# Kernel optimization log

Hardware: AMD Instinct MI355X
Metric: run time of the kernel (lower is better)

Reference implementation:

```python
import jax, jax.numpy as jnp
import numpy as np

B, S, H, A = 2, 512, 256, 128


def setup_inputs() -> dict:
    key = jax.random.key(0)
    k1, k2, k3, k4 = jax.random.split(key, 4)
    x = jax.random.normal(k1, (B, S, H), dtype=jnp.float32)
    attention_mask = jax.random.randint(k2, (B, S), 0, 2, dtype=jnp.int32)
    # xavier_normal for w_a, standard normal for query (as in torch init)
    w_a = jax.random.normal(k3, (H, A), dtype=jnp.float32) * np.sqrt(2.0 / (H + A))
    query = jax.random.normal(k4, (A,), dtype=jnp.float32)
    return {"x": x, "attention_mask": attention_mask, "w_a": w_a, "query": query}


def reference(x, attention_mask, w_a, query):
    # attention_type == 'fixed' path of SelfAttention
    b, s, h = x.shape
    tri = jnp.tril(jnp.ones((s, s), dtype=x.dtype))  # tri[i,j]=1 iff j<=i (causal)
    # values[b,i,j,h] = x[b,j,h] if j<=i else 0  (the O(S^2*H) masked broadcast)
    values = tri[None, :, :, None] * x[:, None, :, :]          # (B,S,S,H)
    key_t = jnp.tanh(jnp.einsum('bijh,ha->bija', values, w_a))  # (B,S,S,A)
    temp = jnp.einsum('a,bija->bij', query, key_t)              # (B,S,S)
    # additive softmax mask: 0 on lower triangle, -inf above diagonal
    smask = jnp.where(tri == 1, 0.0, -jnp.inf).astype(x.dtype)
    d = jax.nn.softmax(temp + smask, axis=-1)                   # (B,S,S)
    am = (attention_mask[:, :s] != 0)
    pair = (am[:, :, None] & am[:, None, :]).astype(d.dtype)    # (B,S,S)
    d = d * pair
    a = jnp.einsum('bij,bjh->bih', d, x)                        # (B,S,H)
    return (a, d)
```

## Files before the change

kernel.cpp:

```cpp
#include <hip/hip_runtime.h>
#include <math.h>

#define BB 2
#define SS 512
#define HH 256
#define AA 128
#define CH 4
#define NCH (SS / CH)

__global__ void k_tc(const float* __restrict__ x,
                     const int* __restrict__ am,
                     const float* __restrict__ w_a,
                     const float* __restrict__ query,
                     float* __restrict__ Ews,
                     float* __restrict__ Cws) {
    const int blk  = blockIdx.x;
    const int b    = blk >> 7;
    const int c    = blk & 127;
    const int j0   = c * CH;
    const int tid  = threadIdx.x;
    const int a    = tid & 127;
    const int half = tid >> 7;

    __shared__ float xs[CH][HH];
    __shared__ float sred[CH][2][AA];
    __shared__ float Wl[CH];

    const float4* xr4 = (const float4*)(x + (size_t)(b * SS + j0) * HH);
    ((float4*)&xs[0][0])[tid] = xr4[tid];
    __syncthreads();

    float acc0 = 0.f, acc1 = 0.f, acc2 = 0.f, acc3 = 0.f;
    const int hbase = half * 128;
    for (int hh = 0; hh < 128; hh += 4) {
        const int h = hbase + hh;
        const float w0 = w_a[(h + 0) * AA + a];
        const float w1 = w_a[(h + 1) * AA + a];
        const float w2 = w_a[(h + 2) * AA + a];
        const float w3 = w_a[(h + 3) * AA + a];
        const float4 x0 = *(const float4*)&xs[0][h];
        const float4 x1 = *(const float4*)&xs[1][h];
        const float4 x2 = *(const float4*)&xs[2][h];
        const float4 x3 = *(const float4*)&xs[3][h];
        acc0 = fmaf(x0.x, w0, fmaf(x0.y, w1, fmaf(x0.z, w2, fmaf(x0.w, w3, acc0))));
        acc1 = fmaf(x1.x, w0, fmaf(x1.y, w1, fmaf(x1.z, w2, fmaf(x1.w, w3, acc1))));
        acc2 = fmaf(x2.x, w0, fmaf(x2.y, w1, fmaf(x2.z, w2, fmaf(x2.w, w3, acc2))));
        acc3 = fmaf(x3.x, w0, fmaf(x3.y, w1, fmaf(x3.z, w2, fmaf(x3.w, w3, acc3))));
    }
    sred[0][half][a] = acc0;
    sred[1][half][a] = acc1;
    sred[2][half][a] = acc2;
    sred[3][half][a] = acc3;
    __syncthreads();

    const int wvi  = tid >> 6;
    const int lane = tid & 63;
    {
        const int r = wvi;
        const float f0 = sred[r][0][lane]      + sred[r][1][lane];
        const float f1 = sred[r][0][lane + 64] + sred[r][1][lane + 64];
        float v = tanhf(f0) * query[lane] + tanhf(f1) * query[lane + 64];
        for (int off = 32; off > 0; off >>= 1)
            v += __shfl_down(v, off, 64);
        if (lane == 0) {
            const float e = expf(v);
            Wl[r] = am[b * SS + j0 + r] ? e : 0.f;
            Ews[b * SS + j0 + r] = e;
        }
    }
    __syncthreads();

    const float cacc = fmaf(Wl[0], xs[0][tid],
                       fmaf(Wl[1], xs[1][tid],
                       fmaf(Wl[2], xs[2][tid],
                            Wl[3] * xs[3][tid])));
    Cws[(size_t)(b * NCH + c) * HH + tid] = cacc;
}

__global__ void k_out(const float* __restrict__ Ews,
                      const float* __restrict__ Cws,
                      const int* __restrict__ am,
                      const float* __restrict__ x,
                      float* __restrict__ dout,
                      float* __restrict__ aout) {
    const int blk  = blockIdx.x;
    const int b    = blk >> 7;
    const int i0   = (blk & 127) << 2;
    const int tid  = threadIdx.x;
    const int lane = tid & 63;
    const int wvi  = tid >> 6;

    __shared__ float Es[SS];
    __shared__ float Ws[SS];
    __shared__ float red[4];
    __shared__ float Pinv[4];

    const float e0 = Ews[b * SS + tid];
    const float e1 = Ews[b * SS + tid + 256];
    const int  am0 = am[b * SS + tid];
    const int  am1 = am[b * SS + tid + 256];
    Es[tid] = e0;             Es[tid + 256] = e1;
    Ws[tid] = am0 ? e0 : 0.f; Ws[tid + 256] = am1 ? e1 : 0.f;

    float p = ((tid <= i0) ? e0 : 0.f) + ((tid + 256 <= i0) ? e1 : 0.f);
    for (int off = 32; off > 0; off >>= 1)
        p += __shfl_down(p, off, 64);
    if (lane == 0) red[wvi] = p;
    __syncthreads();
    if (tid == 0) {
        const float P0 = red[0] + red[1] + red[2] + red[3];
        const float P1 = P0 + Es[i0 + 1];
        const float P2 = P1 + Es[i0 + 2];
        const float P3 = P2 + Es[i0 + 3];
        Pinv[0] = 1.f / P0; Pinv[1] = 1.f / P1;
        Pinv[2] = 1.f / P2; Pinv[3] = 1.f / P3;
    }
    __syncthreads();

    const int* amg = am + b * SS;
    int ami[4];
#pragma unroll
    for (int r = 0; r < 4; ++r) ami[r] = amg[i0 + r];

    const size_t drow = (size_t)(b * SS + i0) * SS;
    const int c4  = tid & 127;
    const int jc  = c4 << 2;
    const float4 wv4 = *(const float4*)&Ws[jc];
#pragma unroll
    for (int pp = 0; pp < 2; ++pp) {
        const int   r  = (tid >> 7) + 2 * pp;
        const int   i  = i0 + r;
        const float pv = Pinv[r];
        const bool  on = ami[r] != 0;
        float4 o;
        o.x = (on && jc + 0 <= i) ? wv4.x * pv : 0.f;
        o.y = (on && jc + 1 <= i) ? wv4.y * pv : 0.f;
        o.z = (on && jc + 2 <= i) ? wv4.z * pv : 0.f;
        o.w = (on && jc + 3 <= i) ? wv4.w * pv : 0.f;
        *(float4*)&dout[drow + (size_t)r * SS + jc] = o;
    }

    const int nfull = i0 >> 2;
    const float* xb = x + (size_t)b * SS * HH + tid;
    const float* Cb = Cws + (size_t)b * NCH * HH + tid;

    float s0 = 0.f, s1 = 0.f, s2 = 0.f, s3 = 0.f;
    int cc = 0;
    for (; cc + 4 <= nfull; cc += 4) {
        s0 += Cb[(size_t)(cc + 0) * HH];
        s1 += Cb[(size_t)(cc + 1) * HH];
        s2 += Cb[(size_t)(cc + 2) * HH];
        s3 += Cb[(size_t)(cc + 3) * HH];
    }
    for (; cc < nfull; ++cc)
        s0 += Cb[(size_t)cc * HH];
    const float base = (s0 + s1) + (s2 + s3);

    const float a0v = fmaf(Ws[i0],     xb[(size_t)(i0)     * HH], base);
    const float a1v = fmaf(Ws[i0 + 1], xb[(size_t)(i0 + 1) * HH], a0v);
    const float a2v = fmaf(Ws[i0 + 2], xb[(size_t)(i0 + 2) * HH], a1v);
    const float a3v = fmaf(Ws[i0 + 3], xb[(size_t)(i0 + 3) * HH], a2v);

    const size_t arow = (size_t)(b * SS + i0) * HH + tid;
    const float av[4] = {a0v, a1v, a2v, a3v};
#pragma unroll
    for (int r = 0; r < 4; ++r)
        aout[arow + (size_t)r * HH] = ami[r] ? av[r] * Pinv[r] : 0.f;
}

extern "C" void kernel_launch(void* const* d_in, const int* in_sizes, int n_in,
                              void* d_out, int out_size, void* d_ws, size_t ws_size,
                              hipStream_t stream) {
    const float* x     = (const float*)d_in[0];
    const int*   am    = (const int*)d_in[1];
    const float* w_a   = (const float*)d_in[2];
    const float* query = (const float*)d_in[3];

    float* a_out  = (float*)d_out;
    float* d_outp = a_out + (size_t)BB * SS * HH;

    float* Ews = (float*)d_ws;
    float* Cws = Ews + BB * SS;

    k_tc <<<BB * NCH,    256, 0, stream>>>(x, am, w_a, query, Ews, Cws);
    k_out<<<BB * SS / 4, 256, 0, stream>>>(Ews, Cws, am, x, d_outp, a_out);
}
```

Baseline: 74.84 us.

## Fuse both kernels into one cooperative kernel with grid-wide prefix scans

Merges the projection kernel and the output kernel into a single cooperative launch of 256 blocks, separated by two grid syncs. Between the syncs, wavefronts compute parallel prefix sums over the chunk partial context vectors and over the exp weights. The output stage then reads one prefix value instead of looping over all earlier chunks and doing a per-block reduction for the softmax denominator. It also drops the shared-memory staging of x in favour of direct global float4 loads. In exchange it adds grid-sync overhead, depends on cooperative launch co-residency, and computes the denominator by prefix summation, which changes the floating-point ordering.

```diff
diff --git a/kernel.cpp b/kernel.cpp
--- a/kernel.cpp
+++ b/kernel.cpp
@@ -1,5 +1,8 @@
 #include <hip/hip_runtime.h>
+#include <hip/hip_cooperative_groups.h>
 #include <math.h>
+
+namespace cg = cooperative_groups;
 
 #define BB 2
 #define SS 512
@@ -8,164 +11,183 @@
 #define CH 4
 #define NCH (SS / CH)
 
-__global__ void k_tc(const float* __restrict__ x,
-                     const int* __restrict__ am,
-                     const float* __restrict__ w_a,
-                     const float* __restrict__ query,
-                     float* __restrict__ Ews,
-                     float* __restrict__ Cws) {
+__global__ __launch_bounds__(256)
+void k_all(const float* __restrict__ x,
+           const int* __restrict__ am,
+           const float* __restrict__ w_a,
+           const float* __restrict__ query,
+           float* __restrict__ Ews,
+           float* __restrict__ Cws,
+           float* __restrict__ Pws,
+           float* __restrict__ dout,
+           float* __restrict__ aout)
+{
+    cg::grid_group grid = cg::this_grid();
     const int blk  = blockIdx.x;
-    const int b    = blk >> 7;
-    const int c    = blk & 127;
-    const int j0   = c * CH;
-    const int tid  = threadIdx.x;
-    const int a    = tid & 127;
-    const int half = tid >> 7;
-
-    __shared__ float xs[CH][HH];
-    __shared__ float sred[CH][2][AA];
-    __shared__ float Wl[CH];
-
-    const float4* xr4 = (const float4*)(x + (size_t)(b * SS + j0) * HH);
-    ((float4*)&xs[0][0])[tid] = xr4[tid];
-    __syncthreads();
-
-    float acc0 = 0.f, acc1 = 0.f, acc2 = 0.f, acc3 = 0.f;
-    const int hbase = half * 128;
-    for (int hh = 0; hh < 128; hh += 4) {
-        const int h = hbase + hh;
-        const float w0 = w_a[(h + 0) * AA + a];
-        const float w1 = w_a[(h + 1) * AA + a];
-        const float w2 = w_a[(h + 2) * AA + a];
-        const float w3 = w_a[(h + 3) * AA + a];
-        const float4 x0 = *(const float4*)&xs[0][h];
-        const float4 x1 = *(const float4*)&xs[1][h];
-        const float4 x2 = *(const float4*)&xs[2][h];
-        const float4 x3 = *(const float4*)&xs[3][h];
-        acc0 = fmaf(x0.x, w0, fmaf(x0.y, w1, fmaf(x0.z, w2, fmaf(x0.w, w3, acc0))));
-        acc1 = fmaf(x1.x, w0, fmaf(x1.y, w1, fmaf(x1.z, w2, fmaf(x1.w, w3, acc1))));
-        acc2 = fmaf(x2.x, w0, fmaf(x2.y, w1, fmaf(x2.z, w2, fmaf(x2.w, w3, acc2))));
-        acc3 = fmaf(x3.x, w0, fmaf(x3.y, w1, fmaf(x3.z, w2, fmaf(x3.w, w3, acc3))));
-    }
-    sred[0][half][a] = acc0;
-    sred[1][half][a] = acc1;
-    sred[2][half][a] = acc2;
-    sred[3][half][a] = acc3;
-    __syncthreads();
-
-    const int wvi  = tid >> 6;
-    const int lane = tid & 63;
-    {
-        const int r = wvi;
-        const float f0 = sred[r][0][lane]      + sred[r][1][lane];
-        const float f1 = sred[r][0][lane + 64] + sred[r][1][lane + 64];
-        float v = tanhf(f0) * query[lane] + tanhf(f1) * query[lane + 64];
-        for (int off = 32; off > 0; off >>= 1)
-            v += __shfl_down(v, off, 64);
-        if (lane == 0) {
-            const float e = expf(v);
-            Wl[r] = am[b * SS + j0 + r] ? e : 0.f;
-            Ews[b * SS + j0 + r] = e;
-        }
-    }
-    __syncthreads();
-
-    const float cacc = fmaf(Wl[0], xs[0][tid],
-                       fmaf(Wl[1], xs[1][tid],
-                       fmaf(Wl[2], xs[2][tid],
-                            Wl[3] * xs[3][tid])));
-    Cws[(size_t)(b * NCH + c) * HH + tid] = cacc;
-}
-
-__global__ void k_out(const float* __restrict__ Ews,
-                      const float* __restrict__ Cws,
-                      const int* __restrict__ am,
-                      const float* __restrict__ x,
-                      float* __restrict__ dout,
-                      float* __restrict__ aout) {
-    const int blk  = blockIdx.x;
-    const int b    = blk >> 7;
-    const int i0   = (blk & 127) << 2;
     const int tid  = threadIdx.x;
     const int lane = tid & 63;
     const int wvi  = tid >> 6;
 
-    __shared__ float Es[SS];
-    __shared__ float Ws[SS];
-    __shared__ float red[4];
-    __shared__ float Pinv[4];
-
-    const float e0 = Ews[b * SS + tid];
-    const float e1 = Ews[b * SS + tid + 256];
-    const int  am0 = am[b * SS + tid];
-    const int  am1 = am[b * SS + tid + 256];
-    Es[tid] = e0;             Es[tid + 256] = e1;
-    Ws[tid] = am0 ? e0 : 0.f; Ws[tid + 256] = am1 ? e1 : 0.f;
-
-    float p = ((tid <= i0) ? e0 : 0.f) + ((tid + 256 <= i0) ? e1 : 0.f);
-    for (int off = 32; off > 0; off >>= 1)
-        p += __shfl_down(p, off, 64);
-    if (lane == 0) red[wvi] = p;
-    __syncthreads();
-    if (tid == 0) {
-        const float P0 = red[0] + red[1] + red[2] + red[3];
-        const float P1 = P0 + Es[i0 + 1];
-        const float P2 = P1 + Es[i0 + 2];
-        const float P3 = P2 + Es[i0 + 3];
-        Pinv[0] = 1.f / P0; Pinv[1] = 1.f / P1;
-        Pinv[2] = 1.f / P2; Pinv[3] = 1.f / P3;
+    __shared__ __align__(16) float sred[CH][2][AA];
+    __shared__ float Wl[CH];
+    __shared__ __align__(16) float Ws[SS];
+
+    {
+        const int b    = blk >> 7;
+        const int c    = blk & 127;
+        const int j0   = c * CH;
+        const int a    = tid & 127;
+        const int half = tid >> 7;
+        const int hbase = __builtin_amdgcn_readfirstlane(half) * 128;
+        const float* xr = x + (size_t)(b * SS + j0) * HH;
+
+        float acc0 = 0.f, acc1 = 0.f, acc2 = 0.f, acc3 = 0.f;
+        for (int hh = 0; hh < 128; hh += 4) {
+            const int h = hbase + hh;
+            const float w0 = w_a[(h + 0) * AA + a];
+            const float w1 = w_a[(h + 1) * AA + a];
+            const float w2 = w_a[(h + 2) * AA + a];
+            const float w3 = w_a[(h + 3) * AA + a];
+            const float4 x0 = *(const float4*)&xr[0 * HH + h];
+            const float4 x1 = *(const float4*)&xr[1 * HH + h];
+            const float4 x2 = *(const float4*)&xr[2 * HH + h];
+            const float4 x3 = *(const float4*)&xr[3 * HH + h];
+            acc0 = fmaf(x0.x, w0, fmaf(x0.y, w1, fmaf(x0.z, w2, fmaf(x0.w, w3, acc0))));
+            acc1 = fmaf(x1.x, w0, fmaf(x1.y, w1, fmaf(x1.z, w2, fmaf(x1.w, w3, acc1))));
+            acc2 = fmaf(x2.x, w0, fmaf(x2.y, w1, fmaf(x2.z, w2, fmaf(x2.w, w3, acc2))));
+            acc3 = fmaf(x3.x, w0, fmaf(x3.y, w1, fmaf(x3.z, w2, fmaf(x3.w, w3, acc3))));
+        }
+        sred[0][half][a] = acc0;
+        sred[1][half][a] = acc1;
+        sred[2][half][a] = acc2;
+        sred[3][half][a] = acc3;
+        __syncthreads();
+
+        {
+            const int r = wvi;
+            const float f0 = sred[r][0][lane]      + sred[r][1][lane];
+            const float f1 = sred[r][0][lane + 64] + sred[r][1][lane + 64];
+            float v = tanhf(f0) * query[lane] + tanhf(f1) * query[lane + 64];
+            for (int off = 32; off > 0; off >>= 1)
+                v += __shfl_down(v, off, 64);
+            if (lane == 0) {
+                const float e = expf(v);
+                Wl[r] = am[b * SS + j0 + r] ? e : 0.f;
+                Ews[b * SS + j0 + r] = e;
+            }
+        }
+        __syncthreads();
+
+        const float cacc = fmaf(Wl[0], xr[0 * HH + tid],
+                           fmaf(Wl[1], xr[1 * HH + tid],
+                           fmaf(Wl[2], xr[2 * HH + tid],
+                                Wl[3] * xr[3 * HH + tid])));
+        Cws[(size_t)(b * NCH + c) * HH + tid] = cacc;
     }
-    __syncthreads();
-
-    const int* amg = am + b * SS;
-    int ami[4];
+
+    __threadfence();
+    grid.sync();
+    __threadfence();
+
+    {
+        const int gw = blk * 4 + wvi;
+        if (gw < 512) {
+            const int b = gw >> 8;
+            const int h = gw & 255;
+            float* Cb = Cws + (size_t)b * NCH * HH + h;
+            const float v0 = Cb[(size_t)(2 * lane)     * HH];
+            const float v1 = Cb[(size_t)(2 * lane + 1) * HH];
+            float p = v0 + v1;
+            for (int off = 1; off < 64; off <<= 1) {
+                const float up = __shfl_up(p, off, 64);
+                if (lane >= off) p += up;
+            }
+            Cb[(size_t)(2 * lane)     * HH] = p - v1;
+            Cb[(size_t)(2 * lane + 1) * HH] = p;
+        } else if (gw < 514) {
+            const int b = gw - 512;
+            const float4 fa = *(const float4*)&Ews[b * SS + lane * 8];
+            const float4 fb = *(const float4*)&Ews[b * SS + lane * 8 + 4];
+            float c0 = fa.x;
+            float c1 = c0 + fa.y;
+            float c2 = c1 + fa.z;
+            float c3 = c2 + fa.w;
+            float c4 = c3 + fb.x;
+            float c5 = c4 + fb.y;
+            float c6 = c5 + fb.z;
+            float c7 = c6 + fb.w;
+            float tot = c7;
+            for (int off = 1; off < 64; off <<= 1) {
+                const float up = __shfl_up(tot, off, 64);
+                if (lane >= off) tot += up;
+            }
+            const float base = tot - c7;
+            float4 oa, ob;
+            oa.x = base + c0; oa.y = base + c1; oa.z = base + c2; oa.w = base + c3;
+            ob.x = base + c4; ob.y = base + c5; ob.z = base + c6; ob.w = base + c7;
+            *(float4*)&Pws[b * SS + lane * 8]     = oa;
+            *(float4*)&Pws[b * SS + lane * 8 + 4] = ob;
+        }
+    }
+
+    __threadfence();
+    grid.sync();
+    __threadfence();
+
+    {
+        const int b  = blk >> 7;
+        const int i0 = (blk & 127) << 2;
+
+        const float e0 = Ews[b * SS + tid];
+        const float e1 = Ews[b * SS + tid + 256];
+        const int  am0 = am[b * SS + tid];
+        const int  am1 = am[b * SS + tid + 256];
+        Ws[tid]       = am0 ? e0 : 0.f;
+        Ws[tid + 256] = am1 ? e1 : 0.f;
+        __syncthreads();
+
+        int   ami[4];
+        float pinv[4];
 #pragma unroll
-    for (int r = 0; r < 4; ++r) ami[r] = amg[i0 + r];
-
-    const size_t drow = (size_t)(b * SS + i0) * SS;
-    const int c4  = tid & 127;
-    const int jc  = c4 << 2;
-    const float4 wv4 = *(const float4*)&Ws[jc];
+        for (int r = 0; r < 4; ++r) {
+            ami[r]  = am[b * SS + i0 + r];
+            pinv[r] = 1.f / Pws[b * SS + i0 + r];
+        }
+
+        const size_t drow = (size_t)(b * SS + i0) * SS;
+        const int c4 = tid & 127;
+        const int jc = c4 << 2;
+        const float4 wv4 = *(const float4*)&Ws[jc];
 #pragma unroll
-    for (int pp = 0; pp < 2; ++pp) {
-        const int   r  = (tid >> 7) + 2 * pp;
-        const int   i  = i0 + r;
-        const float pv = Pinv[r];
-        const bool  on = ami[r] != 0;
-        float4 o;
-        o.x = (on && jc + 0 <= i) ? wv4.x * pv : 0.f;
-        o.y = (on && jc + 1 <= i) ? wv4.y * pv : 0.f;
-        o.z = (on && jc + 2 <= i) ? wv4.z * pv : 0.f;
-        o.w = (on && jc + 3 <= i) ? wv4.w * pv : 0.f;
-        *(float4*)&dout[drow + (size_t)r * SS + jc] = o;
+        for (int pp = 0; pp < 2; ++pp) {
+            const int   r  = (tid >> 7) + 2 * pp;
+            const int   i  = i0 + r;
+            const float pv = pinv[r];
+            const bool  on = ami[r] != 0;
+            float4 o;
+            o.x = (on && jc + 0 <= i) ? wv4.x * pv : 0.f;
+            o.y = (on && jc + 1 <= i) ? wv4.y * pv : 0.f;
+            o.z = (on && jc + 2 <= i) ? wv4.z * pv : 0.f;
+            o.w = (on && jc + 3 <= i) ? wv4.w * pv : 0.f;
+            *(float4*)&dout[drow + (size_t)r * SS + jc] = o;
+        }
+
+        const int nfull = i0 >> 2;
+        const float* xb = x + (size_t)b * SS * HH + tid;
+        const float base = nfull
+            ? Cws[(size_t)(b * NCH + nfull - 1) * HH + tid] : 0.f;
+
+        const float a0v = fmaf(Ws[i0],     xb[(size_t)(i0)     * HH], base);
+        const float a1v = fmaf(Ws[i0 + 1], xb[(size_t)(i0 + 1) * HH], a0v);
+        const float a2v = fmaf(Ws[i0 + 2], xb[(size_t)(i0 + 2) * HH], a1v);
+        const float a3v = fmaf(Ws[i0 + 3], xb[(size_t)(i0 + 3) * HH], a2v);
+
+        const size_t arow = (size_t)(b * SS + i0) * HH + tid;
+        const float av[4] = {a0v, a1v, a2v, a3v};
+#pragma unroll
+        for (int r = 0; r < 4; ++r)
+            aout[arow + (size_t)r * HH] = ami[r] ? av[r] * pinv[r] : 0.f;
     }
-
-    const int nfull = i0 >> 2;
-    const float* xb = x + (size_t)b * SS * HH + tid;
-    const float* Cb = Cws + (size_t)b * NCH * HH + tid;
-
-    float s0 = 0.f, s1 = 0.f, s2 = 0.f, s3 = 0.f;
-    int cc = 0;
-    for (; cc + 4 <= nfull; cc += 4) {
-        s0 += Cb[(size_t)(cc + 0) * HH];
-        s1 += Cb[(size_t)(cc + 1) * HH];
-        s2 += Cb[(size_t)(cc + 2) * HH];
-        s3 += Cb[(size_t)(cc + 3) * HH];
-    }
-    for (; cc < nfull; ++cc)
-        s0 += Cb[(size_t)cc * HH];
-    const float base = (s0 + s1) + (s2 + s3);
-
-    const float a0v = fmaf(Ws[i0],     xb[(size_t)(i0)     * HH], base);
-    const float a1v = fmaf(Ws[i0 + 1], xb[(size_t)(i0 + 1) * HH], a0v);
-    const float a2v = fmaf(Ws[i0 + 2], xb[(size_t)(i0 + 2) * HH], a1v);
-    const float a3v = fmaf(Ws[i0 + 3], xb[(size_t)(i0 + 3) * HH], a2v);
-
-    const size_t arow = (size_t)(b * SS + i0) * HH + tid;
-    const float av[4] = {a0v, a1v, a2v, a3v};
-#pragma unroll
-    for (int r = 0; r < 4; ++r)
-        aout[arow + (size_t)r * HH] = ami[r] ? av[r] * Pinv[r] : 0.f;
 }
 
 extern "C" void kernel_launch(void* const* d_in, const int* in_sizes, int n_in,
@@ -181,7 +203,11 @@
 
     float* Ews = (float*)d_ws;
     float* Cws = Ews + BB * SS;
-
-    k_tc <<<BB * NCH,    256, 0, stream>>>(x, am, w_a, query, Ews, Cws);
-    k_out<<<BB * SS / 4, 256, 0, stream>>>(Ews, Cws, am, x, d_outp, a_out);
+    float* Pws = Cws + (size_t)BB * NCH * HH;
+
+    void* args[] = { (void*)&x, (void*)&am, (void*)&w_a, (void*)&query,
+                     (void*)&Ews, (void*)&Cws, (void*)&Pws,
+                     (void*)&d_outp, (void*)&a_out };
+    hipLaunchCooperativeKernel((const void*)k_all, dim3(BB * NCH), dim3(256),
+                               args, 0, stream);
 }
```

Measured after the change: 214.5 us. 2.87x slower.
